# Performance work log

Hardware: AMD Instinct MI355X
Metric: run time of the kernel (lower is better)

The kernel has to match this reference:

```python
import jax, jax.numpy as jnp
import numpy as np

N_NODES = 100000
N_EDGES = 1600000
FEAT = 128
EMB = 32
N_GRAPHS = 512


def gcn_conv(x, W, b, src, dst, deg_inv_sqrt):
    # PyG GCNConv: h = x @ W; propagate with norm = d_i^{-1/2} d_j^{-1/2} over A + I
    h = x @ W  # [N, out]
    norm = deg_inv_sqrt[src] * deg_inv_sqrt[dst]  # [E]
    msg = h[src] * norm[:, None]  # gather + scale
    agg = jax.ops.segment_sum(msg, dst, num_segments=N_NODES)
    # self-loop contribution: norm_ii = d_i^{-1}
    agg = agg + h * (deg_inv_sqrt * deg_inv_sqrt)[:, None]
    return agg + b


def setup_inputs() -> dict:
    key = jax.random.key(0)
    ks = jax.random.split(key, 10)
    x = jax.random.normal(ks[0], (N_NODES, FEAT), dtype=jnp.float32)
    edge_index = jax.random.randint(ks[1], (2, N_EDGES), 0, N_NODES, dtype=jnp.int64)
    batch_index = jnp.sort(jax.random.randint(ks[2], (N_NODES,), 0, N_GRAPHS, dtype=jnp.int64))
    # Glorot-ish init for weights (PyG GCNConv lin has no bias arg here but conv bias exists)
    def glorot(k, fan_in, fan_out):
        s = jnp.sqrt(6.0 / (fan_in + fan_out)).astype(jnp.float32)
        return jax.random.uniform(k, (fan_in, fan_out), jnp.float32, -s, s)
    W1 = glorot(ks[3], FEAT, EMB)
    b1 = jnp.zeros((EMB,), jnp.float32)
    W2 = glorot(ks[4], EMB, EMB)
    b2 = jnp.zeros((EMB,), jnp.float32)
    Wo = glorot(ks[5], EMB, 1)
    bo = jnp.zeros((1,), jnp.float32)
    return {"x": x, "edge_index": edge_index, "batch_index": batch_index,
            "W1": W1, "b1": b1, "W2": W2, "b2": b2, "Wo": Wo, "bo": bo}


def reference(x, edge_index, batch_index, W1, b1, W2, b2, Wo, bo):
    src, dst = edge_index[0], edge_index[1]
    # degree over A + I (edge weights = 1, counted on dst as in PyG)
    deg = jax.ops.segment_sum(jnp.ones((N_EDGES,), x.dtype), dst, num_segments=N_NODES) + 1.0
    deg_inv_sqrt = jax.lax.rsqrt(deg)

    out = jax.nn.relu(gcn_conv(x, W1, b1, src, dst, deg_inv_sqrt))
    out = jax.nn.relu(gcn_conv(out, W2, b2, src, dst, deg_inv_sqrt))

    # global mean pool over graphs
    summed = jax.ops.segment_sum(out, batch_index, num_segments=N_GRAPHS)  # [G, EMB]
    counts = jax.ops.segment_sum(jnp.ones((N_NODES,), x.dtype), batch_index, num_segments=N_GRAPHS)
    pooled = summed / jnp.maximum(counts, 1.0)[:, None]

    return pooled @ Wo + bo  # [G, 1]
```

## Files before the change

kernel.cpp:

```cpp
#include <hip/hip_runtime.h>
#include <hip/hip_fp16.h>

#define N_NODES 100000
#define N_EDGES 1600000
#define N_GRAPHS 512
#define FEAT 128
#define EMB 32
#define ZROW N_NODES
#define PADCAP (N_EDGES + 8 * N_NODES)
#define NCOPY 64
#define NBKT 250
#define NPB 400
#define ABLK 1024
#define EPB 1563
#define NTILE (N_NODES / 16)

typedef unsigned short u16;
typedef unsigned int u32;
typedef _Float16 f16;
typedef float f32x4 __attribute__((ext_vector_type(4)));
typedef unsigned short u16x4 __attribute__((ext_vector_type(4)));
typedef f16 f16x8 __attribute__((ext_vector_type(8)));

__device__ __forceinline__ int pad8(int d) { return (d + 7) & ~7; }

__device__ __forceinline__ float4 h4_to_f4(u16x4 v) {
  union { unsigned int u; __half2 h; } a, b;
  a.u = (unsigned int)v.x | ((unsigned int)v.y << 16);
  b.u = (unsigned int)v.z | ((unsigned int)v.w << 16);
  float2 f0 = __half22float2(a.h);
  float2 f1 = __half22float2(b.h);
  return make_float4(f0.x, f0.y, f1.x, f1.y);
}

__device__ __forceinline__ u16x4 f4_to_h4(float4 f) {
  union { unsigned int u; __half2 h; } a, b;
  a.h = __float22half2_rn(make_float2(f.x, f.y));
  b.h = __float22half2_rn(make_float2(f.z, f.w));
  u16x4 r;
  r.x = (u16)(a.u & 0xffff); r.y = (u16)(a.u >> 16);
  r.z = (u16)(b.u & 0xffff); r.w = (u16)(b.u >> 16);
  return r;
}


__global__ __launch_bounds__(256) void k_node_init(const int* __restrict__ degcnt,
                                                   float* __restrict__ dis,
                                                   u16* __restrict__ hs1) {
  int i = blockIdx.x * 256 + threadIdx.x;
  if (i < N_NODES) dis[i] = rsqrtf((float)degcnt[i] + 1.0f);
  if (i < EMB) hs1[(size_t)ZROW * EMB + i] = 0;
}

__global__ __launch_bounds__(512) void k_gcnt(const int* __restrict__ batch,
                                              int* __restrict__ gcnt) {
  __shared__ int first[N_GRAPHS + 1];
  int g = threadIdx.x;
  int lo = 0, hi = N_NODES;
  while (lo < hi) {
    int mid = (lo + hi) >> 1;
    if (batch[mid] < g) lo = mid + 1; else hi = mid;
  }
  first[g] = lo;
  if (g == 0) first[N_GRAPHS] = N_NODES;
  __syncthreads();
  gcnt[g] = first[g + 1] - first[g];
}


__global__ __launch_bounds__(256) void k_scanA(const int* __restrict__ degcnt,
                                               int* __restrict__ blocksum) {
  __shared__ int sh[256];
  int t = threadIdx.x;
  int base = blockIdx.x * 1024;
  int s = 0;
#pragma unroll
  for (int j = 0; j < 4; j++) {
    int idx = base + t * 4 + j;
    if (idx < N_NODES) s += pad8(degcnt[idx]);
  }
  sh[t] = s;
  __syncthreads();
  for (int off = 128; off > 0; off >>= 1) {
    if (t < off) sh[t] += sh[t + off];
    __syncthreads();
  }
  if (t == 0) blocksum[blockIdx.x] = sh[0];
}

__global__ __launch_bounds__(128) void k_scanB(const int* __restrict__ blocksum,
                                               int* __restrict__ blockoff,
                                               int* __restrict__ total_out, int nb) {
  __shared__ int sh[128];
  int t = threadIdx.x;
  int v = (t < nb) ? blocksum[t] : 0;
  sh[t] = v;
  __syncthreads();
  for (int off = 1; off < 128; off <<= 1) {
    int add = (t >= off) ? sh[t - off] : 0;
    __syncthreads();
    sh[t] += add;
    __syncthreads();
  }
  if (t < nb) blockoff[t] = sh[t] - v;
  if (t == nb - 1) total_out[0] = sh[t];
}

__global__ __launch_bounds__(256) void k_scanC(const int* __restrict__ degcnt,
                                               const int* __restrict__ blockoff,
                                               int* __restrict__ row_ptr) {
  __shared__ int sh[256];
  int t = threadIdx.x;
  int base = blockIdx.x * 1024;
  int v[4];
#pragma unroll
  for (int j = 0; j < 4; j++) {
    int idx = base + t * 4 + j;
    v[j] = (idx < N_NODES) ? pad8(degcnt[idx]) : 0;
  }
  int tsum = v[0] + v[1] + v[2] + v[3];
  sh[t] = tsum;
  __syncthreads();
  for (int off = 1; off < 256; off <<= 1) {
    int add = (t >= off) ? sh[t - off] : 0;
    __syncthreads();
    sh[t] += add;
    __syncthreads();
  }
  int p = sh[t] - tsum + blockoff[blockIdx.x];
#pragma unroll
  for (int j = 0; j < 4; j++) {
    int idx = base + t * 4 + j;
    if (idx < N_NODES) row_ptr[idx] = p;
    p += v[j];
  }
}


__global__ __launch_bounds__(256) void k_binA(const int* __restrict__ dst,
                                              int* __restrict__ cnt) {
  __shared__ int h[NBKT];
  int k = blockIdx.x, t = threadIdx.x;
  for (int i = t; i < NBKT; i += 256) h[i] = 0;
  __syncthreads();
  int e0 = k * EPB;
  int e1 = min(e0 + EPB, N_EDGES);
  for (int e = e0 + t; e < e1; e += 256)
    atomicAdd(&h[(u32)dst[e] / (u32)NPB], 1);
  __syncthreads();
  for (int i = t; i < NBKT; i += 256) cnt[k * NBKT + i] = h[i];
}

__global__ __launch_bounds__(256) void k_binscanA(const int* __restrict__ cnt,
                                                  int* __restrict__ off,
                                                  int* __restrict__ tot) {
  __shared__ int sh[256];
  int b = blockIdx.x, t = threadIdx.x;
  int v[4];
#pragma unroll
  for (int j = 0; j < 4; j++) v[j] = cnt[(t * 4 + j) * NBKT + b];
  int tsum = v[0] + v[1] + v[2] + v[3];
  sh[t] = tsum;
  __syncthreads();
  for (int o = 1; o < 256; o <<= 1) {
    int add = (t >= o) ? sh[t - o] : 0;
    __syncthreads();
    sh[t] += add;
    __syncthreads();
  }
  int p = sh[t] - tsum;
#pragma unroll
  for (int j = 0; j < 4; j++) {
    off[(t * 4 + j) * NBKT + b] = p;
    p += v[j];
  }
  if (t == 255) tot[b] = p;
}

__global__ __launch_bounds__(256) void k_binscanB(const int* __restrict__ tot,
                                                  int* __restrict__ base) {
  __shared__ int sh[256];
  int t = threadIdx.x;
  int v = (t < NBKT) ? tot[t] : 0;
  sh[t] = v;
  __syncthreads();
  for (int o = 1; o < 256; o <<= 1) {
    int add = (t >= o) ? sh[t - o] : 0;
    __syncthreads();
    sh[t] += add;
    __syncthreads();
  }
  if (t < NBKT) base[t] = sh[t] - v;
  if (t == NBKT - 1) base[NBKT] = sh[t];
}

__global__ __launch_bounds__(256) void k_binscat(const int* __restrict__ src,
                                                 const int* __restrict__ dst,
                                                 const int* __restrict__ off,
                                                 const int* __restrict__ base,
                                                 u32* __restrict__ binbuf) {
  __shared__ int posB[NBKT];
  __shared__ int h[NBKT];
  int k = blockIdx.x, t = threadIdx.x;
  for (int i = t; i < NBKT; i += 256) {
    posB[i] = base[i] + off[k * NBKT + i];
    h[i] = 0;
  }
  __syncthreads();
  int e0 = k * EPB;
  int e1 = min(e0 + EPB, N_EDGES);
  for (int e = e0 + t; e < e1; e += 256) {
    u32 d = (u32)dst[e];
    int b = d / (u32)NPB;
    int r = atomicAdd(&h[b], 1);
    binbuf[posB[b] + r] = (u32)src[e] * (u32)NPB + (d - (u32)b * NPB);
  }
}

__global__ __launch_bounds__(256) void k_bdeg(const u32* __restrict__ binbuf,
                                              const int* __restrict__ base,
                                              int* __restrict__ degcnt) {
  __shared__ int c[NPB];
  int b = blockIdx.x, t = threadIdx.x;
  for (int i = t; i < NPB; i += 256) c[i] = 0;
  __syncthreads();
  int s0 = base[b], s1 = base[b + 1];
  for (int i = s0 + t; i < s1; i += 256) {
    u32 p = binbuf[i];
    u32 s = p / (u32)NPB;
    atomicAdd(&c[p - s * (u32)NPB], 1);
  }
  __syncthreads();
  for (int i = t; i < NPB; i += 256) degcnt[b * NPB + i] = c[i];
}

__global__ __launch_bounds__(256) void k_fillB(const u32* __restrict__ binbuf,
                                               const int* __restrict__ base,
                                               const int* __restrict__ row_ptr,
                                               int* __restrict__ col) {
  __shared__ int rp[NPB + 1];
  __shared__ int cur[NPB];
  int b = blockIdx.x, t = threadIdx.x;
  for (int i = t; i < NPB + 1; i += 256) rp[i] = row_ptr[b * NPB + i];
  for (int i = t; i < NPB; i += 256) cur[i] = 0;
  __syncthreads();
  int s0 = base[b], s1 = base[b + 1];
  for (int i = s0 + t; i < s1; i += 256) {
    u32 p = binbuf[i];
    u32 s = p / (u32)NPB;
    int ld = p - s * (u32)NPB;
    int pos = atomicAdd(&cur[ld], 1);
    col[rp[ld] + pos] = (int)s;
  }
  __syncthreads();
  for (int ld = t; ld < NPB; ld += 256) {
    int bs = rp[ld], len = rp[ld + 1] - bs, c = cur[ld];
    for (int j = c; j < len; j++) col[bs + j] = ZROW;
  }
}


__global__ __launch_bounds__(256) void k_gemm1(const float* __restrict__ x,
                                               const float* __restrict__ W1,
                                               const float* __restrict__ dis,
                                               u16* __restrict__ hs1) {
  int wid = (blockIdx.x * 256 + threadIdx.x) >> 6;
  if (wid >= NTILE) return;
  int l = threadIdx.x & 63;
  int m = l & 15, q = l >> 4;
  f16x8 B[4][2];
#pragma unroll
  for (int s = 0; s < 4; ++s)
#pragma unroll
    for (int h = 0; h < 2; ++h)
#pragma unroll
      for (int j = 0; j < 8; ++j)
        B[s][h][j] = (f16)W1[(s * 32 + q * 8 + j) * EMB + h * 16 + m];
  int row = wid * 16 + m;
  const float* xr = x + (size_t)row * FEAT + q * 8;
  f32x4 acc0 = {0.f, 0.f, 0.f, 0.f}, acc1 = {0.f, 0.f, 0.f, 0.f};
#pragma unroll
  for (int s = 0; s < 4; ++s) {
    f32x4 xa = __builtin_nontemporal_load((const f32x4*)(xr + s * 32));
    f32x4 xb = __builtin_nontemporal_load((const f32x4*)(xr + s * 32 + 4));
    f16x8 A;
    A[0] = (f16)xa.x; A[1] = (f16)xa.y; A[2] = (f16)xa.z; A[3] = (f16)xa.w;
    A[4] = (f16)xb.x; A[5] = (f16)xb.y; A[6] = (f16)xb.z; A[7] = (f16)xb.w;
    acc0 = __builtin_amdgcn_mfma_f32_16x16x32_f16(A, B[s][0], acc0, 0, 0, 0);
    acc1 = __builtin_amdgcn_mfma_f32_16x16x32_f16(A, B[s][1], acc1, 0, 0, 0);
  }
  f32x4 dq = *(const f32x4*)(dis + wid * 16 + q * 4);
  u16* o = hs1 + (size_t)(wid * 16) * EMB;
#pragma unroll
  for (int i = 0; i < 4; ++i) {
    int r = q * 4 + i;
    float dv = (i == 0) ? dq.x : (i == 1) ? dq.y : (i == 2) ? dq.z : dq.w;
    o[(size_t)r * EMB + m]      = __half_as_ushort(__float2half_rn(acc0[i] * dv));
    o[(size_t)r * EMB + 16 + m] = __half_as_ushort(__float2half_rn(acc1[i] * dv));
  }
}

__global__ __launch_bounds__(256) void k_gemm2(const u16* __restrict__ in1,
                                               const float* __restrict__ W2,
                                               const float* __restrict__ dis,
                                               u16* __restrict__ hs2) {
  int wid = (blockIdx.x * 256 + threadIdx.x) >> 6;
  if (wid >= NTILE) return;
  int l = threadIdx.x & 63;
  int m = l & 15, q = l >> 4;
  f16x8 B[2];
#pragma unroll
  for (int h = 0; h < 2; ++h)
#pragma unroll
    for (int j = 0; j < 8; ++j)
      B[h][j] = (f16)W2[(q * 8 + j) * EMB + h * 16 + m];
  int row = wid * 16 + m;
  f16x8 A = *(const f16x8*)(in1 + (size_t)row * EMB + q * 8);
  f32x4 acc0 = {0.f, 0.f, 0.f, 0.f}, acc1 = {0.f, 0.f, 0.f, 0.f};
  acc0 = __builtin_amdgcn_mfma_f32_16x16x32_f16(A, B[0], acc0, 0, 0, 0);
  acc1 = __builtin_amdgcn_mfma_f32_16x16x32_f16(A, B[1], acc1, 0, 0, 0);
  f32x4 dq = *(const f32x4*)(dis + wid * 16 + q * 4);
  u16* o = hs2 + (size_t)(wid * 16) * EMB;
#pragma unroll
  for (int i = 0; i < 4; ++i) {
    int r = q * 4 + i;
    float dv = (i == 0) ? dq.x : (i == 1) ? dq.y : (i == 2) ? dq.z : dq.w;
    o[(size_t)r * EMB + m]      = __half_as_ushort(__float2half_rn(acc0[i] * dv));
    o[(size_t)r * EMB + 16 + m] = __half_as_ushort(__float2half_rn(acc1[i] * dv));
  }
}


__device__ __forceinline__ void agg_two(const u16* __restrict__ hs,
                                        const int* __restrict__ row_ptr,
                                        const int* __restrict__ col,
                                        int n0, int n1, int g, int sub,
                                        float4& R0, float4& R1) {
  const u16x4* hs4 = (const u16x4*)hs;
  int a0 = row_ptr[n0], a1 = row_ptr[n0 + 1];
  int b0 = row_ptr[n1], b1 = row_ptr[n1 + 1];
  int na = (a1 - a0) >> 3, nb = (b1 - b0) >> 3;
  int nch = max(na, nb);
  int eca = a0 + g, ecb = b0 + g;
  float4 A = make_float4(0.f, 0.f, 0.f, 0.f);
  float4 B = make_float4(0.f, 0.f, 0.f, 0.f);
  int sa0 = (0 < na) ? __builtin_nontemporal_load(&col[eca])     : ZROW;
  int sa1 = (1 < na) ? __builtin_nontemporal_load(&col[eca + 8]) : ZROW;
  int sb0 = (0 < nb) ? __builtin_nontemporal_load(&col[ecb])     : ZROW;
  int sb1 = (1 < nb) ? __builtin_nontemporal_load(&col[ecb + 8]) : ZROW;
  for (int i = 0; i < nch; i += 2) {
    u16x4 va0 = hs4[(size_t)sa0 * 8 + sub];
    u16x4 va1 = hs4[(size_t)sa1 * 8 + sub];
    u16x4 vb0 = hs4[(size_t)sb0 * 8 + sub];
    u16x4 vb1 = hs4[(size_t)sb1 * 8 + sub];
    int ta0 = (i + 2 < na) ? __builtin_nontemporal_load(&col[eca + (i + 2) * 8]) : ZROW;
    int ta1 = (i + 3 < na) ? __builtin_nontemporal_load(&col[eca + (i + 3) * 8]) : ZROW;
    int tb0 = (i + 2 < nb) ? __builtin_nontemporal_load(&col[ecb + (i + 2) * 8]) : ZROW;
    int tb1 = (i + 3 < nb) ? __builtin_nontemporal_load(&col[ecb + (i + 3) * 8]) : ZROW;
    float4 fa0 = h4_to_f4(va0), fa1 = h4_to_f4(va1);
    float4 fb0 = h4_to_f4(vb0), fb1 = h4_to_f4(vb1);
    A.x += fa0.x + fa1.x; A.y += fa0.y + fa1.y;
    A.z += fa0.z + fa1.z; A.w += fa0.w + fa1.w;
    B.x += fb0.x + fb1.x; B.y += fb0.y + fb1.y;
    B.z += fb0.z + fb1.z; B.w += fb0.w + fb1.w;
    sa0 = ta0; sa1 = ta1; sb0 = tb0; sb1 = tb1;
  }
#pragma unroll
  for (int mm = 8; mm < 64; mm <<= 1) {
    A.x += __shfl_xor(A.x, mm); A.y += __shfl_xor(A.y, mm);
    A.z += __shfl_xor(A.z, mm); A.w += __shfl_xor(A.w, mm);
    B.x += __shfl_xor(B.x, mm); B.y += __shfl_xor(B.y, mm);
    B.z += __shfl_xor(B.z, mm); B.w += __shfl_xor(B.w, mm);
  }
  float4 s0 = h4_to_f4(hs4[(size_t)n0 * 8 + sub]);
  float4 s1 = h4_to_f4(hs4[(size_t)n1 * 8 + sub]);
  A.x += s0.x; A.y += s0.y; A.z += s0.z; A.w += s0.w;
  B.x += s1.x; B.y += s1.y; B.z += s1.z; B.w += s1.w;
  R0 = A; R1 = B;
}

__device__ __forceinline__ float4 relu_row(float4 acc, float d, float4 bq) {
  float4 o;
  o.x = fmaxf(fmaf(acc.x, d, bq.x), 0.f);
  o.y = fmaxf(fmaf(acc.y, d, bq.y), 0.f);
  o.z = fmaxf(fmaf(acc.z, d, bq.z), 0.f);
  o.w = fmaxf(fmaf(acc.w, d, bq.w), 0.f);
  return o;
}

__global__ __launch_bounds__(256) void k_agg1(const u16* __restrict__ hs,
                                              const int* __restrict__ row_ptr,
                                              const int* __restrict__ col,
                                              const float* __restrict__ dis,
                                              const float* __restrict__ b,
                                              u16* __restrict__ out) {
  int t = threadIdx.x;
  int wv = t >> 6, l = t & 63;
  int n0 = blockIdx.x * 8 + wv * 2, n1 = n0 + 1;
  int g = (l >> 3), sub = l & 7;
  float4 A, B;
  agg_two(hs, row_ptr, col, n0, n1, g, sub, A, B);
  if (g == 0) {
    float4 bq = ((const float4*)b)[sub];
    float4 o0 = relu_row(A, dis[n0], bq);
    float4 o1 = relu_row(B, dis[n1], bq);
    ((u16x4*)(out + (size_t)n0 * EMB))[sub] = f4_to_h4(o0);
    ((u16x4*)(out + (size_t)n1 * EMB))[sub] = f4_to_h4(o1);
  }
}

__global__ __launch_bounds__(256) void k_agg2pool(const u16* __restrict__ hs,
                                                  const int* __restrict__ row_ptr,
                                                  const int* __restrict__ col,
                                                  const float* __restrict__ dis,
                                                  const float* __restrict__ b2,
                                                  const float* __restrict__ Wo,
                                                  const int* __restrict__ batch,
                                                  float* __restrict__ gaccP) {
  int t = threadIdx.x;
  int wv = t >> 6, l = t & 63;
  int n0 = blockIdx.x * 8 + wv * 2, n1 = n0 + 1;
  int g = (l >> 3), sub = l & 7;
  float4 A, B;
  agg_two(hs, row_ptr, col, n0, n1, g, sub, A, B);
  float4 bq = ((const float4*)b2)[sub];
  float4 wq = ((const float4*)Wo)[sub];
  float4 o0 = relu_row(A, dis[n0], bq);
  float4 o1 = relu_row(B, dis[n1], bq);
  float p0 = o0.x * wq.x + o0.y * wq.y + o0.z * wq.z + o0.w * wq.w;
  float p1 = o1.x * wq.x + o1.y * wq.y + o1.z * wq.z + o1.w * wq.w;
  p0 += __shfl_xor(p0, 1); p1 += __shfl_xor(p1, 1);
  p0 += __shfl_xor(p0, 2); p1 += __shfl_xor(p1, 2);
  p0 += __shfl_xor(p0, 4); p1 += __shfl_xor(p1, 4);
  int copy = blockIdx.x & (NCOPY - 1);
  if (l == 0) atomicAdd(&gaccP[copy * N_GRAPHS + batch[n0]], p0);
  if (l == 8) atomicAdd(&gaccP[copy * N_GRAPHS + batch[n1]], p1);
}

__global__ __launch_bounds__(256) void k_finalize(const float* __restrict__ gaccP,
                                                  const int* __restrict__ gcnt,
                                                  const float* __restrict__ bo,
                                                  float* __restrict__ out) {
  int g = blockIdx.x * 256 + threadIdx.x;
  if (g < N_GRAPHS) {
    float s = 0.f;
#pragma unroll 8
    for (int c = 0; c < NCOPY; ++c) s += gaccP[c * N_GRAPHS + g];
    out[g] = s / fmaxf((float)gcnt[g], 1.0f) + bo[0];
  }
}


extern "C" void kernel_launch(void* const* d_in, const int* in_sizes, int n_in,
                              void* d_out, int out_size, void* d_ws, size_t ws_size,
                              hipStream_t stream) {
  const float* x     = (const float*)d_in[0];
  const int*   ei    = (const int*)d_in[1];
  const int*   batch = (const int*)d_in[2];
  const float* W1    = (const float*)d_in[3];
  const float* b1    = (const float*)d_in[4];
  const float* W2    = (const float*)d_in[5];
  const float* b2    = (const float*)d_in[6];
  const float* Wo    = (const float*)d_in[7];
  const float* bo    = (const float*)d_in[8];
  float* out = (float*)d_out;

  const int* src = ei;
  const int* dst = ei + N_EDGES;

  char* w = (char*)d_ws;
  float* gaccP   = (float*)w;  w += (size_t)NCOPY * N_GRAPHS * 4;
  size_t zero_bytes = (size_t)(w - (char*)d_ws);
  int*   degcnt  = (int*)w;    w += (size_t)N_NODES * 4;
  int*   gcnt    = (int*)w;    w += (size_t)N_GRAPHS * 4;
  int*   row_ptr = (int*)w;    w += (size_t)(N_NODES + 4) * 4;
  int*   blocksum= (int*)w;    w += 128 * 4;
  int*   blockoff= (int*)w;    w += 128 * 4;
  int*   cnt     = (int*)w;    w += (size_t)ABLK * NBKT * 4;
  int*   boff    = (int*)w;    w += (size_t)ABLK * NBKT * 4;
  int*   btot    = (int*)w;    w += (size_t)(NBKT + 8) * 4;
  int*   bbase   = (int*)w;    w += (size_t)(NBKT + 8) * 4;
  int*   col     = (int*)w;    w += (size_t)PADCAP * 4;
  float* dis     = (float*)w;  w += (size_t)N_NODES * 4;
  u16*   hs1     = (u16*)w;    w += (size_t)(N_NODES + 1) * EMB * 2;
  u16*   out1    = (u16*)w;    w += (size_t)N_NODES * EMB * 2;
  u32*   binbuf  = (u32*)out1;
  u16*   hs2     = hs1;

  const int NB  = (N_NODES + 255) / 256;
  const int SB  = (N_NODES + 1023) / 1024;
  const int GB  = (NTILE * 64 + 255) / 256;
  const int AB2 = N_NODES / 8;

  (void)hipMemsetAsync(d_ws, 0, zero_bytes, stream);

  k_binA<<<ABLK, 256, 0, stream>>>(dst, cnt);
  k_binscanA<<<NBKT, 256, 0, stream>>>(cnt, boff, btot);
  k_binscanB<<<1, 256, 0, stream>>>(btot, bbase);
  k_binscat<<<ABLK, 256, 0, stream>>>(src, dst, boff, bbase, binbuf);
  k_bdeg<<<NBKT, 256, 0, stream>>>(binbuf, bbase, degcnt);

  k_node_init<<<NB, 256, 0, stream>>>(degcnt, dis, hs1);
  k_gcnt<<<1, 512, 0, stream>>>(batch, gcnt);
  k_scanA<<<SB, 256, 0, stream>>>(degcnt, blocksum);
  k_scanB<<<1, 128, 0, stream>>>(blocksum, blockoff, row_ptr + N_NODES, SB);
  k_scanC<<<SB, 256, 0, stream>>>(degcnt, blockoff, row_ptr);
  k_fillB<<<NBKT, 256, 0, stream>>>(binbuf, bbase, row_ptr, col);

  k_gemm1<<<GB, 256, 0, stream>>>(x, W1, dis, hs1);
  k_agg1<<<AB2, 256, 0, stream>>>(hs1, row_ptr, col, dis, b1, out1);
  k_gemm2<<<GB, 256, 0, stream>>>(out1, W2, dis, hs2);
  k_agg2pool<<<AB2, 256, 0, stream>>>(hs2, row_ptr, col, dis, b2, Wo, batch, gaccP);
  k_finalize<<<2, 256, 0, stream>>>(gaccP, gcnt, bo, out);
}
```

Baseline: 260.0 us.

## Split feature tables into two 16-column halves and aggregate each half separately

Stores hs1/out1/hs2 as two separate 16-feature planes (low and high halves) instead of 32-wide rows. The aggregation kernels now launch twice as many blocks, and each half-wave gathers 32-byte rows from a single half-table with 4-deep unrolled neighbor prefetch. The goal is a smaller gather working set per pass, so each half-table (~3.2MB) stays cache-resident and gather locality improves. The cost is reading the CSR index arrays twice, issuing twice as many atomics in the pooling kernel, and making smaller per-lane memory transactions.

Result: slower. 277.9 us (+6.9%).

```diff
diff --git a/kernel.cpp b/kernel.cpp
--- a/kernel.cpp
+++ b/kernel.cpp
@@ -14,6 +14,8 @@
 #define ABLK 1024
 #define EPB 1563
 #define NTILE (N_NODES / 16)
+#define ABHALF (N_NODES / 8)
+#define HSTRIDE ((size_t)(N_NODES + 1) * 16)
 
 typedef unsigned short u16;
 typedef unsigned int u32;
@@ -49,7 +51,10 @@
                                                    u16* __restrict__ hs1) {
   int i = blockIdx.x * 256 + threadIdx.x;
   if (i < N_NODES) dis[i] = rsqrtf((float)degcnt[i] + 1.0f);
-  if (i < EMB) hs1[(size_t)ZROW * EMB + i] = 0;
+  if (i < 16) {
+    hs1[(size_t)ZROW * 16 + i] = 0;
+    hs1[HSTRIDE + (size_t)ZROW * 16 + i] = 0;
+  }
 }
 
 __global__ __launch_bounds__(512) void k_gcnt(const int* __restrict__ batch,
@@ -290,13 +295,14 @@
     acc1 = __builtin_amdgcn_mfma_f32_16x16x32_f16(A, B[s][1], acc1, 0, 0, 0);
   }
   f32x4 dq = *(const f32x4*)(dis + wid * 16 + q * 4);
-  u16* o = hs1 + (size_t)(wid * 16) * EMB;
+  u16* oL = hs1 + (size_t)(wid * 16) * 16;
+  u16* oH = hs1 + HSTRIDE + (size_t)(wid * 16) * 16;
 #pragma unroll
   for (int i = 0; i < 4; ++i) {
     int r = q * 4 + i;
     float dv = (i == 0) ? dq.x : (i == 1) ? dq.y : (i == 2) ? dq.z : dq.w;
-    o[(size_t)r * EMB + m]      = __half_as_ushort(__float2half_rn(acc0[i] * dv));
-    o[(size_t)r * EMB + 16 + m] = __half_as_ushort(__float2half_rn(acc1[i] * dv));
+    oL[(size_t)r * 16 + m] = __half_as_ushort(__float2half_rn(acc0[i] * dv));
+    oH[(size_t)r * 16 + m] = __half_as_ushort(__float2half_rn(acc1[i] * dv));
   }
 }
 
@@ -315,68 +321,61 @@
     for (int j = 0; j < 8; ++j)
       B[h][j] = (f16)W2[(q * 8 + j) * EMB + h * 16 + m];
   int row = wid * 16 + m;
-  f16x8 A = *(const f16x8*)(in1 + (size_t)row * EMB + q * 8);
+  const u16* ap = in1 + (size_t)(q >> 1) * HSTRIDE + (size_t)row * 16 + (q & 1) * 8;
+  f16x8 A = *(const f16x8*)ap;
   f32x4 acc0 = {0.f, 0.f, 0.f, 0.f}, acc1 = {0.f, 0.f, 0.f, 0.f};
   acc0 = __builtin_amdgcn_mfma_f32_16x16x32_f16(A, B[0], acc0, 0, 0, 0);
   acc1 = __builtin_amdgcn_mfma_f32_16x16x32_f16(A, B[1], acc1, 0, 0, 0);
   f32x4 dq = *(const f32x4*)(dis + wid * 16 + q * 4);
-  u16* o = hs2 + (size_t)(wid * 16) * EMB;
+  u16* oL = hs2 + (size_t)(wid * 16) * 16;
+  u16* oH = hs2 + HSTRIDE + (size_t)(wid * 16) * 16;
 #pragma unroll
   for (int i = 0; i < 4; ++i) {
     int r = q * 4 + i;
     float dv = (i == 0) ? dq.x : (i == 1) ? dq.y : (i == 2) ? dq.z : dq.w;
-    o[(size_t)r * EMB + m]      = __half_as_ushort(__float2half_rn(acc0[i] * dv));
-    o[(size_t)r * EMB + 16 + m] = __half_as_ushort(__float2half_rn(acc1[i] * dv));
-  }
-}
-
-
-__device__ __forceinline__ void agg_two(const u16* __restrict__ hs,
-                                        const int* __restrict__ row_ptr,
-                                        const int* __restrict__ col,
-                                        int n0, int n1, int g, int sub,
-                                        float4& R0, float4& R1) {
-  const u16x4* hs4 = (const u16x4*)hs;
-  int a0 = row_ptr[n0], a1 = row_ptr[n0 + 1];
-  int b0 = row_ptr[n1], b1 = row_ptr[n1 + 1];
-  int na = (a1 - a0) >> 3, nb = (b1 - b0) >> 3;
-  int nch = max(na, nb);
-  int eca = a0 + g, ecb = b0 + g;
+    oL[(size_t)r * 16 + m] = __half_as_ushort(__float2half_rn(acc0[i] * dv));
+    oH[(size_t)r * 16 + m] = __half_as_ushort(__float2half_rn(acc1[i] * dv));
+  }
+}
+
+
+__device__ __forceinline__ float4 agg_half(const u16* __restrict__ tab,
+                                           const int* __restrict__ row_ptr,
+                                           const int* __restrict__ col,
+                                           int node, int g, int sub) {
+  const u16x4* t4 = (const u16x4*)tab;
+  int a0 = row_ptr[node];
+  int na = (row_ptr[node + 1] - a0) >> 3;
+  int ec = a0 + g;
   float4 A = make_float4(0.f, 0.f, 0.f, 0.f);
-  float4 B = make_float4(0.f, 0.f, 0.f, 0.f);
-  int sa0 = (0 < na) ? __builtin_nontemporal_load(&col[eca])     : ZROW;
-  int sa1 = (1 < na) ? __builtin_nontemporal_load(&col[eca + 8]) : ZROW;
-  int sb0 = (0 < nb) ? __builtin_nontemporal_load(&col[ecb])     : ZROW;
-  int sb1 = (1 < nb) ? __builtin_nontemporal_load(&col[ecb + 8]) : ZROW;
-  for (int i = 0; i < nch; i += 2) {
-    u16x4 va0 = hs4[(size_t)sa0 * 8 + sub];
-    u16x4 va1 = hs4[(size_t)sa1 * 8 + sub];
-    u16x4 vb0 = hs4[(size_t)sb0 * 8 + sub];
-    u16x4 vb1 = hs4[(size_t)sb1 * 8 + sub];
-    int ta0 = (i + 2 < na) ? __builtin_nontemporal_load(&col[eca + (i + 2) * 8]) : ZROW;
-    int ta1 = (i + 3 < na) ? __builtin_nontemporal_load(&col[eca + (i + 3) * 8]) : ZROW;
-    int tb0 = (i + 2 < nb) ? __builtin_nontemporal_load(&col[ecb + (i + 2) * 8]) : ZROW;
-    int tb1 = (i + 3 < nb) ? __builtin_nontemporal_load(&col[ecb + (i + 3) * 8]) : ZROW;
-    float4 fa0 = h4_to_f4(va0), fa1 = h4_to_f4(va1);
-    float4 fb0 = h4_to_f4(vb0), fb1 = h4_to_f4(vb1);
-    A.x += fa0.x + fa1.x; A.y += fa0.y + fa1.y;
-    A.z += fa0.z + fa1.z; A.w += fa0.w + fa1.w;
-    B.x += fb0.x + fb1.x; B.y += fb0.y + fb1.y;
-    B.z += fb0.z + fb1.z; B.w += fb0.w + fb1.w;
-    sa0 = ta0; sa1 = ta1; sb0 = tb0; sb1 = tb1;
-  }
-#pragma unroll
-  for (int mm = 8; mm < 64; mm <<= 1) {
+  int s0 = (0 < na) ? __builtin_nontemporal_load(&col[ec])      : ZROW;
+  int s1 = (1 < na) ? __builtin_nontemporal_load(&col[ec + 8])  : ZROW;
+  int s2 = (2 < na) ? __builtin_nontemporal_load(&col[ec + 16]) : ZROW;
+  int s3 = (3 < na) ? __builtin_nontemporal_load(&col[ec + 24]) : ZROW;
+  for (int i = 0; i < na; i += 4) {
+    u16x4 v0 = t4[(size_t)s0 * 4 + sub];
+    u16x4 v1 = t4[(size_t)s1 * 4 + sub];
+    u16x4 v2 = t4[(size_t)s2 * 4 + sub];
+    u16x4 v3 = t4[(size_t)s3 * 4 + sub];
+    s0 = (i + 4 < na) ? __builtin_nontemporal_load(&col[ec + (i + 4) * 8]) : ZROW;
+    s1 = (i + 5 < na) ? __builtin_nontemporal_load(&col[ec + (i + 5) * 8]) : ZROW;
+    s2 = (i + 6 < na) ? __builtin_nontemporal_load(&col[ec + (i + 6) * 8]) : ZROW;
+    s3 = (i + 7 < na) ? __builtin_nontemporal_load(&col[ec + (i + 7) * 8]) : ZROW;
+    float4 f0 = h4_to_f4(v0), f1 = h4_to_f4(v1);
+    float4 f2 = h4_to_f4(v2), f3 = h4_to_f4(v3);
+    A.x += (f0.x + f1.x) + (f2.x + f3.x);
+    A.y += (f0.y + f1.y) + (f2.y + f3.y);
+    A.z += (f0.z + f1.z) + (f2.z + f3.z);
+    A.w += (f0.w + f1.w) + (f2.w + f3.w);
+  }
+#pragma unroll
+  for (int mm = 4; mm < 32; mm <<= 1) {
     A.x += __shfl_xor(A.x, mm); A.y += __shfl_xor(A.y, mm);
     A.z += __shfl_xor(A.z, mm); A.w += __shfl_xor(A.w, mm);
-    B.x += __shfl_xor(B.x, mm); B.y += __shfl_xor(B.y, mm);
-    B.z += __shfl_xor(B.z, mm); B.w += __shfl_xor(B.w, mm);
-  }
-  float4 s0 = h4_to_f4(hs4[(size_t)n0 * 8 + sub]);
-  float4 s1 = h4_to_f4(hs4[(size_t)n1 * 8 + sub]);
-  A.x += s0.x; A.y += s0.y; A.z += s0.z; A.w += s0.w;
-  B.x += s1.x; B.y += s1.y; B.z += s1.z; B.w += s1.w;
-  R0 = A; R1 = B;
+  }
+  float4 s = h4_to_f4(t4[(size_t)node * 4 + sub]);
+  A.x += s.x; A.y += s.y; A.z += s.z; A.w += s.w;
+  return A;
 }
 
 __device__ __forceinline__ float4 relu_row(float4 acc, float d, float4 bq) {
@@ -396,16 +395,18 @@
                                               u16* __restrict__ out) {
   int t = threadIdx.x;
   int wv = t >> 6, l = t & 63;
-  int n0 = blockIdx.x * 8 + wv * 2, n1 = n0 + 1;
-  int g = (l >> 3), sub = l & 7;
-  float4 A, B;
-  agg_two(hs, row_ptr, col, n0, n1, g, sub, A, B);
-  if (g == 0) {
-    float4 bq = ((const float4*)b)[sub];
-    float4 o0 = relu_row(A, dis[n0], bq);
-    float4 o1 = relu_row(B, dis[n1], bq);
-    ((u16x4*)(out + (size_t)n0 * EMB))[sub] = f4_to_h4(o0);
-    ((u16x4*)(out + (size_t)n1 * EMB))[sub] = f4_to_h4(o1);
+  int bid = blockIdx.x;
+  int half = (bid >= ABHALF) ? 1 : 0;
+  int nb = bid - half * ABHALF;
+  int node = nb * 8 + wv * 2 + (l >> 5);
+  int g = (l >> 2) & 7, sub = l & 3;
+  const u16* tab = hs + (size_t)half * HSTRIDE;
+  float4 A = agg_half(tab, row_ptr, col, node, g, sub);
+  if ((l & 31) < 4) {
+    float4 bq = ((const float4*)b)[half * 4 + sub];
+    float4 o = relu_row(A, dis[node], bq);
+    u16x4* dstp = (u16x4*)(out + (size_t)half * HSTRIDE + (size_t)node * 16);
+    __builtin_nontemporal_store(f4_to_h4(o), &dstp[sub]);
   }
 }
 
@@ -419,22 +420,21 @@
                                                   float* __restrict__ gaccP) {
   int t = threadIdx.x;
   int wv = t >> 6, l = t & 63;
-  int n0 = blockIdx.x * 8 + wv * 2, n1 = n0 + 1;
-  int g = (l >> 3), sub = l & 7;
-  float4 A, B;
-  agg_two(hs, row_ptr, col, n0, n1, g, sub, A, B);
-  float4 bq = ((const float4*)b2)[sub];
-  float4 wq = ((const float4*)Wo)[sub];
-  float4 o0 = relu_row(A, dis[n0], bq);
-  float4 o1 = relu_row(B, dis[n1], bq);
-  float p0 = o0.x * wq.x + o0.y * wq.y + o0.z * wq.z + o0.w * wq.w;
-  float p1 = o1.x * wq.x + o1.y * wq.y + o1.z * wq.z + o1.w * wq.w;
-  p0 += __shfl_xor(p0, 1); p1 += __shfl_xor(p1, 1);
-  p0 += __shfl_xor(p0, 2); p1 += __shfl_xor(p1, 2);
-  p0 += __shfl_xor(p0, 4); p1 += __shfl_xor(p1, 4);
-  int copy = blockIdx.x & (NCOPY - 1);
-  if (l == 0) atomicAdd(&gaccP[copy * N_GRAPHS + batch[n0]], p0);
-  if (l == 8) atomicAdd(&gaccP[copy * N_GRAPHS + batch[n1]], p1);
+  int bid = blockIdx.x;
+  int half = (bid >= ABHALF) ? 1 : 0;
+  int nb = bid - half * ABHALF;
+  int node = nb * 8 + wv * 2 + (l >> 5);
+  int g = (l >> 2) & 7, sub = l & 3;
+  const u16* tab = hs + (size_t)half * HSTRIDE;
+  float4 A = agg_half(tab, row_ptr, col, node, g, sub);
+  float4 bq = ((const float4*)b2)[half * 4 + sub];
+  float4 wq = ((const float4*)Wo)[half * 4 + sub];
+  float4 o = relu_row(A, dis[node], bq);
+  float p = o.x * wq.x + o.y * wq.y + o.z * wq.z + o.w * wq.w;
+  p += __shfl_xor(p, 1);
+  p += __shfl_xor(p, 2);
+  int copy = bid & (NCOPY - 1);
+  if ((l & 31) == 0) atomicAdd(&gaccP[copy * N_GRAPHS + batch[node]], p);
 }
 
 __global__ __launch_bounds__(256) void k_finalize(const float* __restrict__ gaccP,
@@ -483,14 +483,14 @@
   int*   col     = (int*)w;    w += (size_t)PADCAP * 4;
   float* dis     = (float*)w;  w += (size_t)N_NODES * 4;
   u16*   hs1     = (u16*)w;    w += (size_t)(N_NODES + 1) * EMB * 2;
-  u16*   out1    = (u16*)w;    w += (size_t)N_NODES * EMB * 2;
+  u16*   out1    = (u16*)w;    w += (size_t)(N_NODES + 1) * EMB * 2;
   u32*   binbuf  = (u32*)out1;
   u16*   hs2     = hs1;
 
   const int NB  = (N_NODES + 255) / 256;
   const int SB  = (N_NODES + 1023) / 1024;
   const int GB  = (NTILE * 64 + 255) / 256;
-  const int AB2 = N_NODES / 8;
+  const int ABG = 2 * ABHALF;
 
   (void)hipMemsetAsync(d_ws, 0, zero_bytes, stream);
 
@@ -508,8 +508,8 @@
   k_fillB<<<NBKT, 256, 0, stream>>>(binbuf, bbase, row_ptr, col);
 
   k_gemm1<<<GB, 256, 0, stream>>>(x, W1, dis, hs1);
-  k_agg1<<<AB2, 256, 0, stream>>>(hs1, row_ptr, col, dis, b1, out1);
+  k_agg1<<<ABG, 256, 0, stream>>>(hs1, row_ptr, col, dis, b1, out1);
   k_gemm2<<<GB, 256, 0, stream>>>(out1, W2, dis, hs2);
-  k_agg2pool<<<AB2, 256, 0, stream>>>(hs2, row_ptr, col, dis, b2, Wo, batch, gaccP);
+  k_agg2pool<<<ABG, 256, 0, stream>>>(hs2, row_ptr, col, dis, b2, Wo, batch, gaccP);
   k_finalize<<<2, 256, 0, stream>>>(gaccP, gcnt, bo, out);
 }
```

## Assign one node per 8-lane group in aggregation and load column indices as int4

Applied to the files above, without the earlier changes.

The aggregation kernels move from one wavefront handling two nodes, with 8 edge-groups per node and a cross-lane shuffle reduction, to each 8-lane group owning a whole node. Each group walks its padded neighbor list sequentially, reading 8 column indices at a time with two vector int4 loads and issuing 8 independent feature gathers per iteration. This removes the cross-group shuffle reduction and the wasted lanes that idle on the shorter of the two paired nodes, and gives four times as many nodes per block. In exchange, each lane runs a serial loop whose length grows with node degree, so high-degree nodes can leave other groups in the wave waiting. The int4 loads also depend on each row's start in col being 8-aligned.

Result: faster. 247.1 us (-4.9%).

```diff
diff --git a/kernel.cpp b/kernel.cpp
--- a/kernel.cpp
+++ b/kernel.cpp
@@ -14,6 +14,7 @@
 #define ABLK 1024
 #define EPB 1563
 #define NTILE (N_NODES / 16)
+#define AGB (N_NODES / 32)
 
 typedef unsigned short u16;
 typedef unsigned int u32;
@@ -331,52 +332,40 @@
 }
 
 
-__device__ __forceinline__ void agg_two(const u16* __restrict__ hs,
-                                        const int* __restrict__ row_ptr,
-                                        const int* __restrict__ col,
-                                        int n0, int n1, int g, int sub,
-                                        float4& R0, float4& R1) {
-  const u16x4* hs4 = (const u16x4*)hs;
-  int a0 = row_ptr[n0], a1 = row_ptr[n0 + 1];
-  int b0 = row_ptr[n1], b1 = row_ptr[n1 + 1];
-  int na = (a1 - a0) >> 3, nb = (b1 - b0) >> 3;
-  int nch = max(na, nb);
-  int eca = a0 + g, ecb = b0 + g;
+__device__ __forceinline__ void acc4(float4& A, u16x4 v) {
+  float4 f = h4_to_f4(v);
+  A.x += f.x; A.y += f.y; A.z += f.z; A.w += f.w;
+}
+
+__device__ __forceinline__ float4 agg_node(const u16* __restrict__ hs,
+                                           const int* __restrict__ row_ptr,
+                                           const int* __restrict__ col,
+                                           int node, int sub) {
+  const u16x4* t4 = (const u16x4*)hs;
+  int a0 = row_ptr[node];
+  int na = row_ptr[node + 1] - a0;
+  const int* cp = col + a0;
+  int4 c0 = *(const int4*)cp;
+  int4 c1 = *(const int4*)(cp + 4);
   float4 A = make_float4(0.f, 0.f, 0.f, 0.f);
-  float4 B = make_float4(0.f, 0.f, 0.f, 0.f);
-  int sa0 = (0 < na) ? __builtin_nontemporal_load(&col[eca])     : ZROW;
-  int sa1 = (1 < na) ? __builtin_nontemporal_load(&col[eca + 8]) : ZROW;
-  int sb0 = (0 < nb) ? __builtin_nontemporal_load(&col[ecb])     : ZROW;
-  int sb1 = (1 < nb) ? __builtin_nontemporal_load(&col[ecb + 8]) : ZROW;
-  for (int i = 0; i < nch; i += 2) {
-    u16x4 va0 = hs4[(size_t)sa0 * 8 + sub];
-    u16x4 va1 = hs4[(size_t)sa1 * 8 + sub];
-    u16x4 vb0 = hs4[(size_t)sb0 * 8 + sub];
-    u16x4 vb1 = hs4[(size_t)sb1 * 8 + sub];
-    int ta0 = (i + 2 < na) ? __builtin_nontemporal_load(&col[eca + (i + 2) * 8]) : ZROW;
-    int ta1 = (i + 3 < na) ? __builtin_nontemporal_load(&col[eca + (i + 3) * 8]) : ZROW;
-    int tb0 = (i + 2 < nb) ? __builtin_nontemporal_load(&col[ecb + (i + 2) * 8]) : ZROW;
-    int tb1 = (i + 3 < nb) ? __builtin_nontemporal_load(&col[ecb + (i + 3) * 8]) : ZROW;
-    float4 fa0 = h4_to_f4(va0), fa1 = h4_to_f4(va1);
-    float4 fb0 = h4_to_f4(vb0), fb1 = h4_to_f4(vb1);
-    A.x += fa0.x + fa1.x; A.y += fa0.y + fa1.y;
-    A.z += fa0.z + fa1.z; A.w += fa0.w + fa1.w;
-    B.x += fb0.x + fb1.x; B.y += fb0.y + fb1.y;
-    B.z += fb0.z + fb1.z; B.w += fb0.w + fb1.w;
-    sa0 = ta0; sa1 = ta1; sb0 = tb0; sb1 = tb1;
-  }
-#pragma unroll
-  for (int mm = 8; mm < 64; mm <<= 1) {
-    A.x += __shfl_xor(A.x, mm); A.y += __shfl_xor(A.y, mm);
-    A.z += __shfl_xor(A.z, mm); A.w += __shfl_xor(A.w, mm);
-    B.x += __shfl_xor(B.x, mm); B.y += __shfl_xor(B.y, mm);
-    B.z += __shfl_xor(B.z, mm); B.w += __shfl_xor(B.w, mm);
-  }
-  float4 s0 = h4_to_f4(hs4[(size_t)n0 * 8 + sub]);
-  float4 s1 = h4_to_f4(hs4[(size_t)n1 * 8 + sub]);
-  A.x += s0.x; A.y += s0.y; A.z += s0.z; A.w += s0.w;
-  B.x += s1.x; B.y += s1.y; B.z += s1.z; B.w += s1.w;
-  R0 = A; R1 = B;
+  for (int i = 0; i < na; i += 8) {
+    u16x4 v0 = t4[(size_t)c0.x * 8 + sub];
+    u16x4 v1 = t4[(size_t)c0.y * 8 + sub];
+    u16x4 v2 = t4[(size_t)c0.z * 8 + sub];
+    u16x4 v3 = t4[(size_t)c0.w * 8 + sub];
+    u16x4 v4 = t4[(size_t)c1.x * 8 + sub];
+    u16x4 v5 = t4[(size_t)c1.y * 8 + sub];
+    u16x4 v6 = t4[(size_t)c1.z * 8 + sub];
+    u16x4 v7 = t4[(size_t)c1.w * 8 + sub];
+    if (i + 8 < na) {
+      c0 = *(const int4*)(cp + i + 8);
+      c1 = *(const int4*)(cp + i + 12);
+    }
+    acc4(A, v0); acc4(A, v1); acc4(A, v2); acc4(A, v3);
+    acc4(A, v4); acc4(A, v5); acc4(A, v6); acc4(A, v7);
+  }
+  acc4(A, t4[(size_t)node * 8 + sub]);
+  return A;
 }
 
 __device__ __forceinline__ float4 relu_row(float4 acc, float d, float4 bq) {
@@ -395,18 +384,13 @@
                                               const float* __restrict__ b,
                                               u16* __restrict__ out) {
   int t = threadIdx.x;
-  int wv = t >> 6, l = t & 63;
-  int n0 = blockIdx.x * 8 + wv * 2, n1 = n0 + 1;
-  int g = (l >> 3), sub = l & 7;
-  float4 A, B;
-  agg_two(hs, row_ptr, col, n0, n1, g, sub, A, B);
-  if (g == 0) {
-    float4 bq = ((const float4*)b)[sub];
-    float4 o0 = relu_row(A, dis[n0], bq);
-    float4 o1 = relu_row(B, dis[n1], bq);
-    ((u16x4*)(out + (size_t)n0 * EMB))[sub] = f4_to_h4(o0);
-    ((u16x4*)(out + (size_t)n1 * EMB))[sub] = f4_to_h4(o1);
-  }
+  int l = t & 63;
+  int node = blockIdx.x * 32 + (t >> 6) * 8 + (l >> 3);
+  int sub = l & 7;
+  float4 A = agg_node(hs, row_ptr, col, node, sub);
+  float4 bq = ((const float4*)b)[sub];
+  float4 o = relu_row(A, dis[node], bq);
+  ((u16x4*)(out + (size_t)node * EMB))[sub] = f4_to_h4(o);
 }
 
 __global__ __launch_bounds__(256) void k_agg2pool(const u16* __restrict__ hs,
@@ -418,23 +402,19 @@
                                                   const int* __restrict__ batch,
                                                   float* __restrict__ gaccP) {
   int t = threadIdx.x;
-  int wv = t >> 6, l = t & 63;
-  int n0 = blockIdx.x * 8 + wv * 2, n1 = n0 + 1;
-  int g = (l >> 3), sub = l & 7;
-  float4 A, B;
-  agg_two(hs, row_ptr, col, n0, n1, g, sub, A, B);
+  int l = t & 63;
+  int node = blockIdx.x * 32 + (t >> 6) * 8 + (l >> 3);
+  int sub = l & 7;
+  float4 A = agg_node(hs, row_ptr, col, node, sub);
   float4 bq = ((const float4*)b2)[sub];
   float4 wq = ((const float4*)Wo)[sub];
-  float4 o0 = relu_row(A, dis[n0], bq);
-  float4 o1 = relu_row(B, dis[n1], bq);
-  float p0 = o0.x * wq.x + o0.y * wq.y + o0.z * wq.z + o0.w * wq.w;
-  float p1 = o1.x * wq.x + o1.y * wq.y + o1.z * wq.z + o1.w * wq.w;
-  p0 += __shfl_xor(p0, 1); p1 += __shfl_xor(p1, 1);
-  p0 += __shfl_xor(p0, 2); p1 += __shfl_xor(p1, 2);
-  p0 += __shfl_xor(p0, 4); p1 += __shfl_xor(p1, 4);
-  int copy = blockIdx.x & (NCOPY - 1);
-  if (l == 0) atomicAdd(&gaccP[copy * N_GRAPHS + batch[n0]], p0);
-  if (l == 8) atomicAdd(&gaccP[copy * N_GRAPHS + batch[n1]], p1);
+  float4 o = relu_row(A, dis[node], bq);
+  float p = o.x * wq.x + o.y * wq.y + o.z * wq.z + o.w * wq.w;
+  p += __shfl_xor(p, 1);
+  p += __shfl_xor(p, 2);
+  p += __shfl_xor(p, 4);
+  if (sub == 0)
+    atomicAdd(&gaccP[(node & (NCOPY - 1)) * N_GRAPHS + batch[node]], p);
 }
 
 __global__ __launch_bounds__(256) void k_finalize(const float* __restrict__ gaccP,
@@ -490,7 +470,6 @@
   const int NB  = (N_NODES + 255) / 256;
   const int SB  = (N_NODES + 1023) / 1024;
   const int GB  = (NTILE * 64 + 255) / 256;
-  const int AB2 = N_NODES / 8;
 
   (void)hipMemsetAsync(d_ws, 0, zero_bytes, stream);
 
@@ -508,8 +487,8 @@
   k_fillB<<<NBKT, 256, 0, stream>>>(binbuf, bbase, row_ptr, col);
 
   k_gemm1<<<GB, 256, 0, stream>>>(x, W1, dis, hs1);
-  k_agg1<<<AB2, 256, 0, stream>>>(hs1, row_ptr, col, dis, b1, out1);
+  k_agg1<<<AGB, 256, 0, stream>>>(hs1, row_ptr, col, dis, b1, out1);
   k_gemm2<<<GB, 256, 0, stream>>>(out1, W2, dis, hs2);
-  k_agg2pool<<<AB2, 256, 0, stream>>>(hs2, row_ptr, col, dis, b2, Wo, batch, gaccP);
+  k_agg2pool<<<AGB, 256, 0, stream>>>(hs2, row_ptr, col, dis, b2, Wo, batch, gaccP);
   k_finalize<<<2, 256, 0, stream>>>(gaccP, gcnt, bo, out);
 }
```
